# Kernel optimization log

Hardware: AMD Instinct MI355X
Metric: run time of the kernel (lower is better)

## Reference

```python
import jax, jax.numpy as jnp
import numpy as np

N_NODES = 100000
N_EDGES = 1600000
MUL = 32            # channel multiplicity for every irrep
INV_SQRT_MUL = 1.0 / np.sqrt(32.0)
# path constants: wigner-3j norms (1/sqrt3 for 0x1->1 and 1x1->0, 1/sqrt6 for 1x1->1)
# combined with fan-in path normalization (fan=32 for 0e out, fan=64 for 1o out, 2 paths)
C_DOT = 1.0 / np.sqrt(3.0 * 32.0)
C_SCL = 1.0 / np.sqrt(3.0 * 64.0)
C_CRS = 1.0 / np.sqrt(6.0 * 64.0)


def setup_inputs() -> dict:
    key = jax.random.key(0)
    ks = jax.random.split(key, 12)
    x = jax.random.normal(ks[0], (N_NODES, 128), jnp.float32)
    pos = jax.random.normal(ks[1], (N_NODES, 3), jnp.float32)
    edge_index = jax.random.randint(ks[2], (2, N_EDGES), 0, N_NODES, jnp.int32)
    # o3.Linear(32x0e+32x1o -> 32x0e+32x0e+32x1o): per-irrep channel mixing
    W_node_s = jax.random.normal(ks[3], (32, 64), jnp.float32)   # 0e -> (scalars|gates)
    W_node_v = jax.random.normal(ks[4], (32, 32), jnp.float32)   # 1o -> 1o
    # FullyConnectedTensorProduct(32x0e+32x1o, 1x1o -> 32x0e+32x1o): 3 CG paths
    W_tp_d = jax.random.normal(ks[5], (32, 32), jnp.float32)     # 1o x 1o -> 0e (dot)
    W_tp_s = jax.random.normal(ks[6], (32, 32), jnp.float32)     # 0e x 1o -> 1o
    W_tp_c = jax.random.normal(ks[7], (32, 32), jnp.float32)     # 1o x 1o -> 1o (cross)
    # o3.Linear(32x0e+32x1o -> 32x0e+32x1o)
    W_msg_s = jax.random.normal(ks[8], (32, 32), jnp.float32)
    W_msg_v = jax.random.normal(ks[9], (32, 32), jnp.float32)
    ln_gamma = jnp.ones((128,), jnp.float32)
    ln_beta = jnp.zeros((128,), jnp.float32)
    return {"x": x, "pos": pos, "edge_index": edge_index,
            "W_node_s": W_node_s, "W_node_v": W_node_v,
            "W_tp_d": W_tp_d, "W_tp_s": W_tp_s, "W_tp_c": W_tp_c,
            "W_msg_s": W_msg_s, "W_msg_v": W_msg_v,
            "ln_gamma": ln_gamma, "ln_beta": ln_beta}


def reference(x, pos, edge_index, W_node_s, W_node_v, W_tp_d, W_tp_s, W_tp_c,
              W_msg_s, W_msg_v, ln_gamma, ln_beta):
    N = x.shape[0]
    row, col = edge_index[0], edge_index[1]
    # split node irreps: 32 scalars (0e) | 32 vectors (1o) of dim 3
    s = x[:, :32]                       # [N,32]
    v = x[:, 32:].reshape(-1, 32, 3)    # [N,32,3]
    # lin_node (equivariant linear, path-normalized by 1/sqrt(fan_in)=1/sqrt(32))
    h_s = (s @ W_node_s) * INV_SQRT_MUL                          # [N,64]
    h_v = jnp.einsum('nid,ij->njd', v, W_node_v) * INV_SQRT_MUL  # [N,32,3]
    # Gate: relu scalars, sigmoid gates multiply the gated vectors
    sc = jax.nn.relu(h_s[:, :32])                                # [N,32]
    hv = h_v * jax.nn.sigmoid(h_s[:, 32:])[:, :, None]           # [N,32,3]
    # spherical harmonics l=1, component norm: sqrt(3)*unit vec in e3nn (y,z,x) order
    rel = pos[col] - pos[row]                                    # [E,3]
    unit = rel / jnp.sqrt(jnp.sum(rel * rel, -1, keepdims=True) + 1e-12)
    u = jnp.sqrt(3.0) * unit[:, (1, 2, 0)]                       # [E,3]
    # gather source-node features per edge
    sj = sc[col]                                                 # [E,32]
    vj = hv[col]                                                 # [E,32,3]
    # CG tensor product paths
    dot = jnp.einsum('eid,ed->ei', vj, u)                        # 1o x 1o -> 0e
    crs = jnp.cross(vj, u[:, None, :])                           # 1o x 1o -> 1o
    m0 = (dot @ W_tp_d) * C_DOT                                  # [E,32]
    m1 = (sj @ W_tp_s)[:, :, None] * u[:, None, :] * C_SCL \
         + jnp.einsum('eid,ik->ekd', crs, W_tp_c) * C_CRS        # [E,32,3]
    m = jnp.concatenate([m0, m1.reshape(-1, 96)], -1)            # [E,128]
    # scatter-mean over destination nodes (row)
    deg = jax.ops.segment_sum(jnp.ones_like(row, jnp.float32), row,
                              num_segments=N).clip(1.0)
    mi = jax.ops.segment_sum(m, row, num_segments=N) / deg[:, None]
    # lin_msg
    ms = (mi[:, :32] @ W_msg_s) * INV_SQRT_MUL
    mv = jnp.einsum('nid,ij->njd', mi[:, 32:].reshape(-1, 32, 3),
                    W_msg_v) * INV_SQRT_MUL
    o = jnp.concatenate([ms, mv.reshape(-1, 96)], -1)            # [N,128]
    # LayerNorm over 128 dims (as in the original, affine)
    mu = o.mean(-1, keepdims=True)
    var = o.var(-1, keepdims=True)
    o = (o - mu) / jnp.sqrt(var + 1e-5) * ln_gamma + ln_beta
    return x + o
```

## Files before the change

kernel.cpp:

```cpp
#include <hip/hip_runtime.h>
#include <math.h>


static constexpr float INV_SQRT_MUL = 0.17677669529663687f;
static constexpr float C_DOT = 0.10206207261596575f;
static constexpr float C_SCL = 0.07216878364870322f;
static constexpr float C_CRS = 0.05103103630798288f;
static constexpr float SQRT3 = 1.7320508075688772f;
static constexpr int MAXDEG = 48;
static constexpr int COMB_B = 2048;
static constexpr int CNT_WORDS = 8 * 16384;

#define WS_ALIGN(x) (((x) + 255) & ~(size_t)255)
#define CIDX(r) ((((r) & 7) << 14) | ((r) >> 3))

__device__ __forceinline__ unsigned short f2bf(float v) {
    unsigned int b = __float_as_uint(v);
    b += 0x7FFFu + ((b >> 16) & 1u);
    return (unsigned short)(b >> 16);
}
__device__ __forceinline__ float bf2f(unsigned short u) {
    return __uint_as_float(((unsigned int)u) << 16);
}

__global__ __launch_bounds__(1024)
void fuse_w(const float* __restrict__ Wns, const float* __restrict__ Wnv,
            const float* __restrict__ Wtpd, const float* __restrict__ Wtps,
            const float* __restrict__ Wtpc, const float* __restrict__ Wms,
            const float* __restrict__ Wmv, float* __restrict__ Wall) {
    int t = threadIdx.x;
    int i = t >> 5, j = t & 31;
    float a = 0.f, b = 0.f, c = 0.f;
#pragma unroll
    for (int k = 0; k < 32; ++k) {
        a += Wtpd[i * 32 + k] * Wms[k * 32 + j];
        b += Wtps[i * 32 + k] * Wmv[k * 32 + j];
        c += Wtpc[i * 32 + k] * Wmv[k * 32 + j];
    }
    Wall[t]        = a * (C_DOT * INV_SQRT_MUL);
    Wall[1024 + t] = b * (C_SCL * INV_SQRT_MUL);
    Wall[2048 + t] = c * (C_CRS * INV_SQRT_MUL);
    int i2 = t >> 5, k2 = t & 31;
    Wall[3072 + t]        = Wns[k2 * 64 + i2];
    Wall[3072 + 1024 + t] = Wns[k2 * 64 + 32 + i2];
    Wall[5120 + t]        = Wnv[k2 * 32 + i2];
}

__global__ __launch_bounds__(256)
void phase1(const float* __restrict__ x, const float* __restrict__ WT,
            const int* __restrict__ eidx, ushort4* __restrict__ feat4,
            int* __restrict__ cnt, int* __restrict__ slots, int N, int E) {
    __shared__ float buf[4][64 * 36];
    int t = threadIdx.x;

    if ((blockIdx.x & 8) == 0) {
        int shard = blockIdx.x & 7;
        int sid = (int)(blockIdx.x >> 4);
        int tid = sid * 256 + t;
        const int SSTRIDE = (COMB_B / 16) * 256;
        int Q = E >> 2;
        const int4* r4p = (const int4*)eidx;
        const int4* c4p = (const int4*)(eidx + E);
        for (int q = tid; q < Q; q += SSTRIDE) {
            int4 R = r4p[q];
            bool any = ((R.x & 7) == shard) | ((R.y & 7) == shard) |
                       ((R.z & 7) == shard) | ((R.w & 7) == shard);
            if (!any) continue;
            int4 C = c4p[q];
            int rr[4] = {R.x, R.y, R.z, R.w};
            int cc[4] = {C.x, C.y, C.z, C.w};
#pragma unroll
            for (int k = 0; k < 4; ++k) {
                if ((rr[k] & 7) == shard) {
                    int p = atomicAdd(&cnt[CIDX(rr[k])], 1);
                    if (p < MAXDEG) slots[(size_t)rr[k] * MAXDEG + p] = cc[k];
                }
            }
        }
        for (int e = (Q << 2) + tid; e < E; e += SSTRIDE) {
            int r = eidx[e];
            if ((r & 7) == shard) {
                int c = eidx[E + e];
                int p = atomicAdd(&cnt[CIDX(r)], 1);
                if (p < MAXDEG) slots[(size_t)r * MAXDEG + p] = c;
            }
        }
    } else {
        int fid = (int)(((blockIdx.x >> 4) << 3) | (blockIdx.x & 7));
        int wv = t >> 6, l = t & 63;
        float* bw = buf[wv];
        int nt = (N + 63) >> 6;
        int r0 = l >> 3, cw = (l & 7) << 2;
        const float* WnsT = WT;
        const float* WnvT = WT + 2048;

        for (int tile = fid * 4 + wv; tile < nt; tile += (COMB_B / 2) * 4) {
            int B = tile << 6;
            auto stage = [&](int w0) {
#pragma unroll
                for (int j = 0; j < 8; ++j) {
                    int row = j * 8 + r0;
                    int node = B + row;
                    float4 v = make_float4(0.f, 0.f, 0.f, 0.f);
                    if (node < N) v = *(const float4*)(x + (size_t)node * 128 + w0 + cw);
                    *(float4*)(bw + row * 36 + cw) = v;
                }
                __builtin_amdgcn_wave_barrier();
            };
            auto readrow = [&](float* dst) {
                const float4* rp = (const float4*)(bw + l * 36);
#pragma unroll
                for (int j = 0; j < 8; ++j) {
                    float4 q = rp[j];
                    dst[4*j] = q.x; dst[4*j+1] = q.y; dst[4*j+2] = q.z; dst[4*j+3] = q.w;
                }
                __builtin_amdgcn_wave_barrier();
            };

            float xs[32];
            stage(0); readrow(xs);
            unsigned int scp[16];
            float sig[32];
#pragma unroll 2
            for (int i = 0; i < 32; ++i) {
                float a = 0.f, g = 0.f;
#pragma unroll
                for (int k = 0; k < 32; ++k) {
                    a += xs[k] * WnsT[i * 32 + k];
                    g += xs[k] * WnsT[(32 + i) * 32 + k];
                }
                a = fmaxf(a * INV_SQRT_MUL, 0.f);
                float s = 1.f / (1.f + __expf(-g * INV_SQRT_MUL));
                unsigned short s16 = f2bf(a);
                if ((i & 1) == 0) scp[i >> 1] = s16;
                else scp[i >> 1] |= ((unsigned int)s16) << 16;
                sig[i] = s * INV_SQRT_MUL;
            }
            float xv[96];
            stage(32); readrow(xv);
            stage(64); readrow(xv + 32);
            stage(96); readrow(xv + 64);
            int node = B + l;
            bool liv = (node < N);
#pragma unroll 2
            for (int i = 0; i < 32; ++i) {
                float o0 = 0.f, o1 = 0.f, o2 = 0.f;
#pragma unroll
                for (int k = 0; k < 32; ++k) {
                    float w = WnvT[i * 32 + k];
                    o0 += xv[3 * k + 0] * w;
                    o1 += xv[3 * k + 1] * w;
                    o2 += xv[3 * k + 2] * w;
                }
                float s = sig[i];
                unsigned int scw = scp[i >> 1];
                ushort4 pk;
                pk.x = (unsigned short)((i & 1) ? (scw >> 16) : (scw & 0xFFFFu));
                pk.y = f2bf(o0 * s); pk.z = f2bf(o1 * s); pk.w = f2bf(o2 * s);
                if (liv) feat4[(size_t)node * 32 + i] = pk;
            }
            __builtin_amdgcn_wave_barrier();
        }
    }
}

__global__ __launch_bounds__(256)
void agg(const float* __restrict__ x, const float* __restrict__ pos,
         const ushort4* __restrict__ feat4, const int* __restrict__ cnt,
         const int* __restrict__ slots, const float* __restrict__ Wall,
         const float* __restrict__ gamma, const float* __restrict__ beta,
         float* __restrict__ out, int N) {
    __shared__ float4 cu[8][MAXDEG];
    __shared__ float4 finA[8][32];
    __shared__ float4 finB[8][32];
    int t = threadIdx.x;
    int hw = t >> 5, lane = t & 31;
    int n = blockIdx.x * 8 + hw;
    bool live = (n < N);
    int nn = live ? n : 0;

    int deg = cnt[CIDX(nn)];
    size_t srow = (size_t)nn * MAXDEG;
    int col0 = slots[srow + lane];
    int col1 = slots[srow + 32 + (lane & 15)];
    float prx = pos[nn * 3 + 0], pry = pos[nn * 3 + 1], prz = pos[nn * 3 + 2];
    if (!live) deg = 0;
    int c = min(deg, MAXDEG);
    int cpad = (c + 3) & ~3;

    if (lane < c) {
        float rx = pos[col0 * 3 + 0] - prx, ry = pos[col0 * 3 + 1] - pry, rz = pos[col0 * 3 + 2] - prz;
        float inv = rsqrtf(rx * rx + ry * ry + rz * rz + 1e-12f) * SQRT3;
        cu[hw][lane] = make_float4(ry * inv, rz * inv, rx * inv, __int_as_float(col0 << 8));
    } else {
        cu[hw][lane] = make_float4(0.f, 0.f, 0.f, __int_as_float(0));
    }
    if (lane < 16) {
        int idx = 32 + lane;
        if (idx < c) {
            float rx = pos[col1 * 3 + 0] - prx, ry = pos[col1 * 3 + 1] - pry, rz = pos[col1 * 3 + 2] - prz;
            float inv = rsqrtf(rx * rx + ry * ry + rz * rz + 1e-12f) * SQRT3;
            cu[hw][idx] = make_float4(ry * inv, rz * inv, rx * inv, __int_as_float(col1 << 8));
        } else {
            cu[hw][idx] = make_float4(0.f, 0.f, 0.f, __int_as_float(0));
        }
    }
    __builtin_amdgcn_wave_barrier();

    const char* featB = (const char*)feat4;
    unsigned int ch8 = (unsigned int)lane * 8u;
    const float4* cuw = cu[hw];
    float D = 0.f, S0 = 0.f, S1 = 0.f, S2 = 0.f, C0 = 0.f, C1 = 0.f, C2 = 0.f;

    for (int jb = 0; jb < cpad; jb += 4) {
        float4 q[4]; ushort4 f[4];
#pragma unroll
        for (int k = 0; k < 4; ++k) q[k] = cuw[jb + k];
#pragma unroll
        for (int k = 0; k < 4; ++k)
            f[k] = *(const ushort4*)(featB + (__float_as_uint(q[k].w) + ch8));
#pragma unroll
        for (int k = 0; k < 4; ++k) {
            float u0 = q[k].x, u1 = q[k].y, u2 = q[k].z;
            float sj = bf2f(f[k].x);
            float h0 = bf2f(f[k].y), h1 = bf2f(f[k].z), h2 = bf2f(f[k].w);
            D  += h0 * u0 + h1 * u1 + h2 * u2;
            S0 += sj * u0; S1 += sj * u1; S2 += sj * u2;
            C0 += h1 * u2 - h2 * u1;
            C1 += h2 * u0 - h0 * u2;
            C2 += h0 * u1 - h1 * u0;
        }
    }

    finA[hw][lane] = make_float4(D, S0, S1, S2);
    finB[hw][lane] = make_float4(C0, C1, C2, 0.f);
    __builtin_amdgcn_wave_barrier();

    float invdeg = 1.0f / (float)((deg > 0) ? deg : 1);
    float a0 = 0.f, aV0 = 0.f, aV1 = 0.f, aV2 = 0.f;
#pragma unroll 8
    for (int i = 0; i < 32; ++i) {
        float4 a = finA[hw][i];
        float4 b = finB[hw][i];
        float wd = Wall[i * 32 + lane];
        float ws = Wall[1024 + i * 32 + lane];
        float wc = Wall[2048 + i * 32 + lane];
        a0  += a.x * wd;
        aV0 += a.y * ws + b.x * wc;
        aV1 += a.z * ws + b.y * wc;
        aV2 += a.w * ws + b.z * wc;
    }
    float vd = a0 * invdeg;
    float v0 = aV0 * invdeg, v1 = aV1 * invdeg, v2 = aV2 * invdeg;

    float s1 = vd + v0 + v1 + v2;
    float s2 = vd * vd + v0 * v0 + v1 * v1 + v2 * v2;
#pragma unroll
    for (int m = 16; m >= 1; m >>= 1) {
        s1 += __shfl_xor(s1, m);
        s2 += __shfl_xor(s2, m);
    }
    float mu = s1 * (1.f / 128.f);
    float var = s2 * (1.f / 128.f) - mu * mu;
    float rstd = rsqrtf(var + 1e-5f);

    if (live) {
        size_t base = (size_t)n * 128;
        int chv = 32 + lane * 3;
        float xv0 = __builtin_nontemporal_load(&x[base + lane]);
        float xa  = __builtin_nontemporal_load(&x[base + chv + 0]);
        float xb  = __builtin_nontemporal_load(&x[base + chv + 1]);
        float xc  = __builtin_nontemporal_load(&x[base + chv + 2]);
        __builtin_nontemporal_store(xv0 + (vd - mu) * rstd * gamma[lane] + beta[lane], &out[base + lane]);
        __builtin_nontemporal_store(xa + (v0 - mu) * rstd * gamma[chv + 0] + beta[chv + 0], &out[base + chv + 0]);
        __builtin_nontemporal_store(xb + (v1 - mu) * rstd * gamma[chv + 1] + beta[chv + 1], &out[base + chv + 1]);
        __builtin_nontemporal_store(xc + (v2 - mu) * rstd * gamma[chv + 2] + beta[chv + 2], &out[base + chv + 2]);
    }
}

extern "C" void kernel_launch(void* const* d_in, const int* in_sizes, int n_in,
                              void* d_out, int out_size, void* d_ws, size_t ws_size,
                              hipStream_t stream) {
    const float* x     = (const float*)d_in[0];
    const float* pos   = (const float*)d_in[1];
    const int*   eidx  = (const int*)d_in[2];
    const float* Wns   = (const float*)d_in[3];
    const float* Wnv   = (const float*)d_in[4];
    const float* Wtpd  = (const float*)d_in[5];
    const float* Wtps  = (const float*)d_in[6];
    const float* Wtpc  = (const float*)d_in[7];
    const float* Wms   = (const float*)d_in[8];
    const float* Wmv   = (const float*)d_in[9];
    const float* gamma = (const float*)d_in[10];
    const float* beta  = (const float*)d_in[11];
    float* out = (float*)d_out;

    int N = in_sizes[0] / 128;
    int E = in_sizes[2] / 2;

    char* ws = (char*)d_ws;
    size_t off = 0;
    unsigned short* feat = (unsigned short*)(ws + off); off += WS_ALIGN((size_t)N * 128 * 2);
    int*   cnt  = (int*)(ws + off);   off += WS_ALIGN((size_t)CNT_WORDS * 4);
    float* Wall = (float*)(ws + off); off += WS_ALIGN(6144 * 4);
    int*   slots = (int*)(ws + off);

    hipMemsetAsync(cnt, 0, (size_t)CNT_WORDS * 4, stream);
    fuse_w<<<1, 1024, 0, stream>>>(Wns, Wnv, Wtpd, Wtps, Wtpc, Wms, Wmv, Wall);
    phase1<<<COMB_B, 256, 0, stream>>>(x, Wall + 3072, eidx, (ushort4*)feat, cnt, slots, N, E);
    agg<<<(N + 7) / 8, 256, 0, stream>>>(x, pos, (const ushort4*)feat, cnt, slots, Wall, gamma, beta, out, N);
}
```

Before: 369.8 us.

## Split fused scatter/node-feature kernel into separate kernels and fold counter zeroing

The combined phase1 kernel, which split its blocks between edge-slot scattering and the node feature linear layer, becomes two kernels. The scatter kernel gives all 2048 blocks to edge bucketing with 8 shards. The node_feat kernel launches one 128-thread block per two 64-node tiles instead of a grid-stride loop. The hipMemsetAsync of the counters is folded into the weight-fusion kernel as extra blocks, removing one launch but serialising the scatter and feature work that previously ran concurrently.

```diff
diff --git a/kernel.cpp b/kernel.cpp
--- a/kernel.cpp
+++ b/kernel.cpp
@@ -8,7 +8,7 @@
 static constexpr float C_CRS = 0.05103103630798288f;
 static constexpr float SQRT3 = 1.7320508075688772f;
 static constexpr int MAXDEG = 48;
-static constexpr int COMB_B = 2048;
+static constexpr int SCAT_B = 2048;
 static constexpr int CNT_WORDS = 8 * 16384;
 
 #define WS_ALIGN(x) (((x) + 255) & ~(size_t)255)
@@ -24,143 +24,146 @@
 }
 
 __global__ __launch_bounds__(1024)
-void fuse_w(const float* __restrict__ Wns, const float* __restrict__ Wnv,
-            const float* __restrict__ Wtpd, const float* __restrict__ Wtps,
-            const float* __restrict__ Wtpc, const float* __restrict__ Wms,
-            const float* __restrict__ Wmv, float* __restrict__ Wall) {
+void fuse_zero(const float* __restrict__ Wns, const float* __restrict__ Wnv,
+               const float* __restrict__ Wtpd, const float* __restrict__ Wtps,
+               const float* __restrict__ Wtpc, const float* __restrict__ Wms,
+               const float* __restrict__ Wmv, float* __restrict__ Wall,
+               int* __restrict__ cnt) {
     int t = threadIdx.x;
-    int i = t >> 5, j = t & 31;
-    float a = 0.f, b = 0.f, c = 0.f;
-#pragma unroll
-    for (int k = 0; k < 32; ++k) {
-        a += Wtpd[i * 32 + k] * Wms[k * 32 + j];
-        b += Wtps[i * 32 + k] * Wmv[k * 32 + j];
-        c += Wtpc[i * 32 + k] * Wmv[k * 32 + j];
-    }
-    Wall[t]        = a * (C_DOT * INV_SQRT_MUL);
-    Wall[1024 + t] = b * (C_SCL * INV_SQRT_MUL);
-    Wall[2048 + t] = c * (C_CRS * INV_SQRT_MUL);
-    int i2 = t >> 5, k2 = t & 31;
-    Wall[3072 + t]        = Wns[k2 * 64 + i2];
-    Wall[3072 + 1024 + t] = Wns[k2 * 64 + 32 + i2];
-    Wall[5120 + t]        = Wnv[k2 * 32 + i2];
+    if (blockIdx.x == 0) {
+        int i = t >> 5, j = t & 31;
+        float a = 0.f, b = 0.f, c = 0.f;
+#pragma unroll
+        for (int k = 0; k < 32; ++k) {
+            a += Wtpd[i * 32 + k] * Wms[k * 32 + j];
+            b += Wtps[i * 32 + k] * Wmv[k * 32 + j];
+            c += Wtpc[i * 32 + k] * Wmv[k * 32 + j];
+        }
+        Wall[t]        = a * (C_DOT * INV_SQRT_MUL);
+        Wall[1024 + t] = b * (C_SCL * INV_SQRT_MUL);
+        Wall[2048 + t] = c * (C_CRS * INV_SQRT_MUL);
+        int i2 = t >> 5, k2 = t & 31;
+        Wall[3072 + t]        = Wns[k2 * 64 + i2];
+        Wall[3072 + 1024 + t] = Wns[k2 * 64 + 32 + i2];
+        Wall[5120 + t]        = Wnv[k2 * 32 + i2];
+    } else {
+        int i = (blockIdx.x - 1) * 1024 + t;
+        if (i < CNT_WORDS) cnt[i] = 0;
+    }
 }
 
 __global__ __launch_bounds__(256)
-void phase1(const float* __restrict__ x, const float* __restrict__ WT,
-            const int* __restrict__ eidx, ushort4* __restrict__ feat4,
-            int* __restrict__ cnt, int* __restrict__ slots, int N, int E) {
-    __shared__ float buf[4][64 * 36];
+void scatter(const int* __restrict__ eidx, int* __restrict__ cnt,
+             int* __restrict__ slots, int E) {
+    int shard = blockIdx.x & 7;
+    int tid = (blockIdx.x >> 3) * 256 + threadIdx.x;
+    const int SSTRIDE = (SCAT_B / 8) * 256;
+    int Q = E >> 2;
+    const int4* r4p = (const int4*)eidx;
+    const int4* c4p = (const int4*)(eidx + E);
+    for (int q = tid; q < Q; q += SSTRIDE) {
+        int4 R = r4p[q];
+        bool any = ((R.x & 7) == shard) | ((R.y & 7) == shard) |
+                   ((R.z & 7) == shard) | ((R.w & 7) == shard);
+        if (!any) continue;
+        int4 C = c4p[q];
+        int rr[4] = {R.x, R.y, R.z, R.w};
+        int cc[4] = {C.x, C.y, C.z, C.w};
+#pragma unroll
+        for (int k = 0; k < 4; ++k) {
+            if ((rr[k] & 7) == shard) {
+                int p = atomicAdd(&cnt[CIDX(rr[k])], 1);
+                if (p < MAXDEG) slots[(size_t)rr[k] * MAXDEG + p] = cc[k];
+            }
+        }
+    }
+    for (int e = (Q << 2) + tid; e < E; e += SSTRIDE) {
+        int r = eidx[e];
+        if ((r & 7) == shard) {
+            int c = eidx[E + e];
+            int p = atomicAdd(&cnt[CIDX(r)], 1);
+            if (p < MAXDEG) slots[(size_t)r * MAXDEG + p] = c;
+        }
+    }
+}
+
+__global__ __launch_bounds__(128)
+void node_feat(const float* __restrict__ x, const float* __restrict__ WT,
+               ushort4* __restrict__ feat4, int N) {
+    __shared__ float buf[2][64 * 36];
     int t = threadIdx.x;
-
-    if ((blockIdx.x & 8) == 0) {
-        int shard = blockIdx.x & 7;
-        int sid = (int)(blockIdx.x >> 4);
-        int tid = sid * 256 + t;
-        const int SSTRIDE = (COMB_B / 16) * 256;
-        int Q = E >> 2;
-        const int4* r4p = (const int4*)eidx;
-        const int4* c4p = (const int4*)(eidx + E);
-        for (int q = tid; q < Q; q += SSTRIDE) {
-            int4 R = r4p[q];
-            bool any = ((R.x & 7) == shard) | ((R.y & 7) == shard) |
-                       ((R.z & 7) == shard) | ((R.w & 7) == shard);
-            if (!any) continue;
-            int4 C = c4p[q];
-            int rr[4] = {R.x, R.y, R.z, R.w};
-            int cc[4] = {C.x, C.y, C.z, C.w};
-#pragma unroll
-            for (int k = 0; k < 4; ++k) {
-                if ((rr[k] & 7) == shard) {
-                    int p = atomicAdd(&cnt[CIDX(rr[k])], 1);
-                    if (p < MAXDEG) slots[(size_t)rr[k] * MAXDEG + p] = cc[k];
-                }
-            }
-        }
-        for (int e = (Q << 2) + tid; e < E; e += SSTRIDE) {
-            int r = eidx[e];
-            if ((r & 7) == shard) {
-                int c = eidx[E + e];
-                int p = atomicAdd(&cnt[CIDX(r)], 1);
-                if (p < MAXDEG) slots[(size_t)r * MAXDEG + p] = c;
-            }
-        }
-    } else {
-        int fid = (int)(((blockIdx.x >> 4) << 3) | (blockIdx.x & 7));
-        int wv = t >> 6, l = t & 63;
-        float* bw = buf[wv];
-        int nt = (N + 63) >> 6;
-        int r0 = l >> 3, cw = (l & 7) << 2;
-        const float* WnsT = WT;
-        const float* WnvT = WT + 2048;
-
-        for (int tile = fid * 4 + wv; tile < nt; tile += (COMB_B / 2) * 4) {
-            int B = tile << 6;
-            auto stage = [&](int w0) {
-#pragma unroll
-                for (int j = 0; j < 8; ++j) {
-                    int row = j * 8 + r0;
-                    int node = B + row;
-                    float4 v = make_float4(0.f, 0.f, 0.f, 0.f);
-                    if (node < N) v = *(const float4*)(x + (size_t)node * 128 + w0 + cw);
-                    *(float4*)(bw + row * 36 + cw) = v;
-                }
-                __builtin_amdgcn_wave_barrier();
-            };
-            auto readrow = [&](float* dst) {
-                const float4* rp = (const float4*)(bw + l * 36);
-#pragma unroll
-                for (int j = 0; j < 8; ++j) {
-                    float4 q = rp[j];
-                    dst[4*j] = q.x; dst[4*j+1] = q.y; dst[4*j+2] = q.z; dst[4*j+3] = q.w;
-                }
-                __builtin_amdgcn_wave_barrier();
-            };
-
-            float xs[32];
-            stage(0); readrow(xs);
-            unsigned int scp[16];
-            float sig[32];
+    int wv = t >> 6, l = t & 63;
+    float* bw = buf[wv];
+    int nt = (N + 63) >> 6;
+    int tile = blockIdx.x * 2 + wv;
+    if (tile >= nt) return;
+    int B = tile << 6;
+    int r0 = l >> 3, cw = (l & 7) << 2;
+    const float* WnsT = WT;
+    const float* WnvT = WT + 2048;
+
+    auto stage = [&](int w0) {
+#pragma unroll
+        for (int j = 0; j < 8; ++j) {
+            int row = j * 8 + r0;
+            int node = B + row;
+            float4 v = make_float4(0.f, 0.f, 0.f, 0.f);
+            if (node < N) v = *(const float4*)(x + (size_t)node * 128 + w0 + cw);
+            *(float4*)(bw + row * 36 + cw) = v;
+        }
+        __builtin_amdgcn_wave_barrier();
+    };
+    auto readrow = [&](float* dst) {
+        const float4* rp = (const float4*)(bw + l * 36);
+#pragma unroll
+        for (int j = 0; j < 8; ++j) {
+            float4 q = rp[j];
+            dst[4*j] = q.x; dst[4*j+1] = q.y; dst[4*j+2] = q.z; dst[4*j+3] = q.w;
+        }
+        __builtin_amdgcn_wave_barrier();
+    };
+
+    float xs[32];
+    stage(0); readrow(xs);
+    unsigned int scp[16];
+    float sig[32];
 #pragma unroll 2
-            for (int i = 0; i < 32; ++i) {
-                float a = 0.f, g = 0.f;
-#pragma unroll
-                for (int k = 0; k < 32; ++k) {
-                    a += xs[k] * WnsT[i * 32 + k];
-                    g += xs[k] * WnsT[(32 + i) * 32 + k];
-                }
-                a = fmaxf(a * INV_SQRT_MUL, 0.f);
-                float s = 1.f / (1.f + __expf(-g * INV_SQRT_MUL));
-                unsigned short s16 = f2bf(a);
-                if ((i & 1) == 0) scp[i >> 1] = s16;
-                else scp[i >> 1] |= ((unsigned int)s16) << 16;
-                sig[i] = s * INV_SQRT_MUL;
-            }
-            float xv[96];
-            stage(32); readrow(xv);
-            stage(64); readrow(xv + 32);
-            stage(96); readrow(xv + 64);
-            int node = B + l;
-            bool liv = (node < N);
+    for (int i = 0; i < 32; ++i) {
+        float a = 0.f, g = 0.f;
+#pragma unroll
+        for (int k = 0; k < 32; ++k) {
+            a += xs[k] * WnsT[i * 32 + k];
+            g += xs[k] * WnsT[(32 + i) * 32 + k];
+        }
+        a = fmaxf(a * INV_SQRT_MUL, 0.f);
+        float s = 1.f / (1.f + __expf(-g * INV_SQRT_MUL));
+        unsigned short s16 = f2bf(a);
+        if ((i & 1) == 0) scp[i >> 1] = s16;
+        else scp[i >> 1] |= ((unsigned int)s16) << 16;
+        sig[i] = s * INV_SQRT_MUL;
+    }
+    float xv[96];
+    stage(32); readrow(xv);
+    stage(64); readrow(xv + 32);
+    stage(96); readrow(xv + 64);
+    int node = B + l;
+    bool liv = (node < N);
 #pragma unroll 2
-            for (int i = 0; i < 32; ++i) {
-                float o0 = 0.f, o1 = 0.f, o2 = 0.f;
-#pragma unroll
-                for (int k = 0; k < 32; ++k) {
-                    float w = WnvT[i * 32 + k];
-                    o0 += xv[3 * k + 0] * w;
-                    o1 += xv[3 * k + 1] * w;
-                    o2 += xv[3 * k + 2] * w;
-                }
-                float s = sig[i];
-                unsigned int scw = scp[i >> 1];
-                ushort4 pk;
-                pk.x = (unsigned short)((i & 1) ? (scw >> 16) : (scw & 0xFFFFu));
-                pk.y = f2bf(o0 * s); pk.z = f2bf(o1 * s); pk.w = f2bf(o2 * s);
-                if (liv) feat4[(size_t)node * 32 + i] = pk;
-            }
-            __builtin_amdgcn_wave_barrier();
-        }
+    for (int i = 0; i < 32; ++i) {
+        float o0 = 0.f, o1 = 0.f, o2 = 0.f;
+#pragma unroll
+        for (int k = 0; k < 32; ++k) {
+            float w = WnvT[i * 32 + k];
+            o0 += xv[3 * k + 0] * w;
+            o1 += xv[3 * k + 1] * w;
+            o2 += xv[3 * k + 2] * w;
+        }
+        float s = sig[i];
+        unsigned int scw = scp[i >> 1];
+        ushort4 pk;
+        pk.x = (unsigned short)((i & 1) ? (scw >> 16) : (scw & 0xFFFFu));
+        pk.y = f2bf(o0 * s); pk.z = f2bf(o1 * s); pk.w = f2bf(o2 * s);
+        if (liv) feat4[(size_t)node * 32 + i] = pk;
     }
 }
 
@@ -305,8 +308,10 @@
     float* Wall = (float*)(ws + off); off += WS_ALIGN(6144 * 4);
     int*   slots = (int*)(ws + off);
 
-    hipMemsetAsync(cnt, 0, (size_t)CNT_WORDS * 4, stream);
-    fuse_w<<<1, 1024, 0, stream>>>(Wns, Wnv, Wtpd, Wtps, Wtpc, Wms, Wmv, Wall);
-    phase1<<<COMB_B, 256, 0, stream>>>(x, Wall + 3072, eidx, (ushort4*)feat, cnt, slots, N, E);
+    int zb = 1 + (CNT_WORDS + 1023) / 1024;
+    fuse_zero<<<zb, 1024, 0, stream>>>(Wns, Wnv, Wtpd, Wtps, Wtpc, Wms, Wmv, Wall, cnt);
+    scatter<<<SCAT_B, 256, 0, stream>>>(eidx, cnt, slots, E);
+    int nt = (N + 63) >> 6;
+    node_feat<<<(nt + 1) / 2, 128, 0, stream>>>(x, Wall + 3072, (ushort4*)feat, N);
     agg<<<(N + 7) / 8, 256, 0, stream>>>(x, pos, (const ushort4*)feat, cnt, slots, Wall, gamma, beta, out, N);
 }
```

Result: faster. 352.3 us (-4.7%).
